# Performance work log

Measured on AMD Instinct MI355X. Metric: run time of the kernel, lower is better.

Reference implementation:

```python
import jax, jax.numpy as jnp
import numpy as np

# Plane-stress elasticity constants (E=1.0, nu=0.3), matching ModelXToResult.__init__
E_MOD = 1.0
NU = 0.3
C11 = E_MOD / (1.0 - NU ** 2)          # = c22
C12 = E_MOD * NU / (1.0 - NU ** 2)     # = c21
C33 = E_MOD / (2.0 * (1.0 + NU))

HIDDEN = 256


def setup_inputs() -> dict:
    key = jax.random.key(0)
    ks = jax.random.split(key, 5)
    B, N = 4, 65536
    X = jax.random.uniform(ks[0], (B, N, 2), dtype=jnp.float32)
    # MLP params (2 -> 256 -> 256 -> 256 -> 2), scaled ~ 1/sqrt(fan_in)
    W1 = jax.random.normal(ks[1], (2, HIDDEN), dtype=jnp.float32) / np.sqrt(2.0)
    b1 = jnp.zeros((HIDDEN,), jnp.float32)
    W2 = jax.random.normal(ks[2], (HIDDEN, HIDDEN), dtype=jnp.float32) / np.sqrt(HIDDEN)
    b2 = jnp.zeros((HIDDEN,), jnp.float32)
    W3 = jax.random.normal(ks[3], (HIDDEN, HIDDEN), dtype=jnp.float32) / np.sqrt(HIDDEN)
    b3 = jnp.zeros((HIDDEN,), jnp.float32)
    Wo = jax.random.normal(ks[4], (HIDDEN, 2), dtype=jnp.float32) / np.sqrt(HIDDEN)
    bo = jnp.zeros((2,), jnp.float32)
    return {"X": X, "W1": W1, "b1": b1, "W2": W2, "b2": b2,
            "W3": W3, "b3": b3, "Wo": Wo, "bo": bo}


def _disp(xy, W1, b1, W2, b2, W3, b3, Wo, bo):
    # xy: [B, N, 2] -> displacement [B, N, 2] = (u, v)
    h = jnp.tanh(xy @ W1 + b1)
    h = jnp.tanh(h @ W2 + b2)
    h = jnp.tanh(h @ W3 + b3)
    return h @ Wo + bo


def reference(X, W1, b1, W2, b2, W3, b3, Wo, bo):
    f = lambda xy: _disp(xy, W1, b1, W2, b2, W3, b3, Wo, bo)
    ones = jnp.ones_like(X[..., 0:1])
    zeros = jnp.zeros_like(ones)
    tx = jnp.concatenate([ones, zeros], axis=-1)  # d/dx tangent
    ty = jnp.concatenate([zeros, ones], axis=-1)  # d/dy tangent
    # Fused forward + full 2x2 Jacobian via two forward-mode JVPs
    out, d_dx = jax.jvp(f, (X,), (tx,))
    _, d_dy = jax.jvp(f, (X,), (ty,))
    u, v = out[..., 0:1], out[..., 1:2]
    u_x, v_x = d_dx[..., 0:1], d_dx[..., 1:2]
    u_y, v_y = d_dy[..., 0:1], d_dy[..., 1:2]
    u_xy = u_y + v_x
    stress_x = C11 * u_x + C12 * v_y
    stress_y = C12 * u_x + C11 * v_y
    stress_xy = C33 * u_xy
    strain_energy_density = 0.5 * (stress_x * u_x + stress_y * v_y + stress_xy * u_xy)
    return (u, v, stress_x, stress_y, stress_xy, strain_energy_density)
```

## Files before the change

### kernel.cpp

```cpp
#include <hip/hip_runtime.h>

#define HIDDEN 256
#define NPTS (4*65536)
#define MTILE 16
#define NWG (NPTS/MTILE)
#define THREADS 256
#define BUF 24576

typedef _Float16 h8  __attribute__((ext_vector_type(8)));
typedef float    f4  __attribute__((ext_vector_type(4)));

__device__ __forceinline__ float2 tanh_ts(float x){
  const float e = exp2f(x * 2.885390081777927f);
  const float r = __builtin_amdgcn_rcpf(e + 1.0f);
  const float t = fmaf(-2.0f, r, 1.0f);
  const float q = 4.0f * r;
  const float s = fmaf(-q, r, q);
  return float2{t, s};
}

__device__ __forceinline__ uint2 pack4(float a, float b, float c, float d){
  uint2 r;
  r.x = __builtin_bit_cast(unsigned int, __builtin_amdgcn_cvt_pkrtz(a, b));
  r.y = __builtin_bit_cast(unsigned int, __builtin_amdgcn_cvt_pkrtz(c, d));
  return r;
}

__device__ __forceinline__ int act_off(int p, int ubyte){
  return p*512 + (ubyte ^ ((p & 15) << 4));
}

__global__ void pack_weights(const float* __restrict__ W, _Float16* __restrict__ dst){
  int i = blockIdx.x * blockDim.x + threadIdx.x;
  int l  = i & 63;
  int nt = (i >> 6) & 15;
  int ks = i >> 10;
  int k0 = ks*32 + ((l >> 4) << 3);
  int n  = nt*16 + (l & 15);
  h8 v;
  #pragma unroll
  for (int j = 0; j < 8; ++j) v[j] = (_Float16)W[(k0 + j)*HIDDEN + n];
  *reinterpret_cast<h8*>(dst + (size_t)i*8) = v;
}

__launch_bounds__(THREADS, 2)
__global__ void pinn_fused(const float* __restrict__ X,
                           const float* __restrict__ W1,
                           const float* __restrict__ b1,
                           const float* __restrict__ b2,
                           const float* __restrict__ b3,
                           const float* __restrict__ Wo,
                           const float* __restrict__ bo,
                           const _Float16* __restrict__ Wp,
                           float* __restrict__ out)
{
  __shared__ __align__(16) char actS[2*BUF];
  __shared__ __align__(16) float partS[MTILE*24];

  const int tid = threadIdx.x;
  const int l   = tid & 63;
  const int lg  = l >> 4;
  const int lr  = l & 15;
  const int Uq  = __builtin_amdgcn_readfirstlane(tid >> 6);

  {
    const int pl = tid & 15;
    const int ug = tid >> 4;
    const int P  = blockIdx.x * MTILE + pl;
    const float2 xy = *reinterpret_cast<const float2*>(X + 2*P);
    #pragma unroll
    for (int c = 0; c < 4; ++c){
      const int u = ug*16 + c*4;
      const f4 w0 = *reinterpret_cast<const f4*>(W1 + u);
      const f4 w1 = *reinterpret_cast<const f4*>(W1 + HIDDEN + u);
      const f4 bb = *reinterpret_cast<const f4*>(b1 + u);
      float h[4], gx[4], gy[4];
      #pragma unroll
      for (int j = 0; j < 4; ++j){
        const float z = fmaf(xy.x, w0[j], fmaf(xy.y, w1[j], bb[j]));
        const float2 ts = tanh_ts(z);
        h[j]  = ts.x;
        gx[j] = ts.y * w0[j];
        gy[j] = ts.y * w1[j];
      }
      const int off = act_off(pl, u*2);
      *reinterpret_cast<uint2*>(actS + 0*8192 + off) = pack4(h[0],h[1],h[2],h[3]);
      *reinterpret_cast<uint2*>(actS + 1*8192 + off) = pack4(gx[0],gx[1],gx[2],gx[3]);
      *reinterpret_cast<uint2*>(actS + 2*8192 + off) = pack4(gy[0],gy[1],gy[2],gy[3]);
    }
  }
  __syncthreads();

  {
    const _Float16* WL = Wp;
    f4 acc[3][4];
    const f4 fzero = {0.f, 0.f, 0.f, 0.f};
    #pragma unroll
    for (int s = 0; s < 3; ++s)
      #pragma unroll
      for (int ut = 0; ut < 4; ++ut) acc[s][ut] = fzero;

    #pragma unroll
    for (int ks = 0; ks < 8; ++ks){
      h8 wf[4];
      #pragma unroll
      for (int ut = 0; ut < 4; ++ut)
        wf[ut] = *reinterpret_cast<const h8*>(WL + (size_t)(((ks*16 + Uq*4 + ut)*64 + l))*8);
      const int off = act_off(lr, ks*64 + lg*16);
      #pragma unroll
      for (int s = 0; s < 3; ++s){
        const h8 af = *reinterpret_cast<const h8*>(actS + s*8192 + off);
        #pragma unroll
        for (int ut = 0; ut < 4; ++ut)
          acc[s][ut] = __builtin_amdgcn_mfma_f32_16x16x32_f16(wf[ut], af, acc[s][ut], 0, 0, 0);
      }
    }

    #pragma unroll
    for (int ut = 0; ut < 4; ++ut){
      const int u0 = Uq*64 + ut*16 + lg*4;
      const f4 bb = *reinterpret_cast<const f4*>(b2 + u0);
      const f4 z  = acc[0][ut];
      const f4 zx = acc[1][ut];
      const f4 zy = acc[2][ut];
      float h[4], gx[4], gy[4];
      #pragma unroll
      for (int j = 0; j < 4; ++j){
        const float2 ts = tanh_ts(z[j] + bb[j]);
        h[j]  = ts.x;
        gx[j] = ts.y * zx[j];
        gy[j] = ts.y * zy[j];
      }
      const int off = act_off(lr, u0*2);
      *reinterpret_cast<uint2*>(actS + BUF + 0*8192 + off) = pack4(h[0],h[1],h[2],h[3]);
      *reinterpret_cast<uint2*>(actS + BUF + 1*8192 + off) = pack4(gx[0],gx[1],gx[2],gx[3]);
      *reinterpret_cast<uint2*>(actS + BUF + 2*8192 + off) = pack4(gy[0],gy[1],gy[2],gy[3]);
    }
  }
  __syncthreads();

  {
    const _Float16* WL = Wp + 65536;
    f4 acc[3][4];
    const f4 fzero = {0.f, 0.f, 0.f, 0.f};
    #pragma unroll
    for (int s = 0; s < 3; ++s)
      #pragma unroll
      for (int ut = 0; ut < 4; ++ut) acc[s][ut] = fzero;

    #pragma unroll
    for (int ks = 0; ks < 8; ++ks){
      h8 wf[4];
      #pragma unroll
      for (int ut = 0; ut < 4; ++ut)
        wf[ut] = *reinterpret_cast<const h8*>(WL + (size_t)(((ks*16 + Uq*4 + ut)*64 + l))*8);
      const int off = act_off(lr, ks*64 + lg*16);
      #pragma unroll
      for (int s = 0; s < 3; ++s){
        const h8 af = *reinterpret_cast<const h8*>(actS + BUF + s*8192 + off);
        #pragma unroll
        for (int ut = 0; ut < 4; ++ut)
          acc[s][ut] = __builtin_amdgcn_mfma_f32_16x16x32_f16(wf[ut], af, acc[s][ut], 0, 0, 0);
      }
    }

    float au=0.f, av=0.f, aux=0.f, avx=0.f, auy=0.f, avy=0.f;
    #pragma unroll
    for (int ut = 0; ut < 4; ++ut){
      const int u0 = Uq*64 + ut*16 + lg*4;
      const f4 bb  = *reinterpret_cast<const f4*>(b3 + u0);
      const f4 wo0 = *reinterpret_cast<const f4*>(Wo + 2*u0);
      const f4 wo1 = *reinterpret_cast<const f4*>(Wo + 2*u0 + 4);
      const f4 z  = acc[0][ut];
      const f4 zx = acc[1][ut];
      const f4 zy = acc[2][ut];
      #pragma unroll
      for (int j = 0; j < 4; ++j){
        const float2 ts = tanh_ts(z[j] + bb[j]);
        const float gx = ts.y * zx[j];
        const float gy = ts.y * zy[j];
        const float wx = (j < 2) ? wo0[2*(j&1)]   : wo1[2*(j&1)];
        const float wy = (j < 2) ? wo0[2*(j&1)+1] : wo1[2*(j&1)+1];
        au  += ts.x*wx;  av  += ts.x*wy;
        aux += gx*wx;    avx += gx*wy;
        auy += gy*wx;    avy += gy*wy;
      }
    }
    #pragma unroll
    for (int m = 16; m <= 32; m <<= 1){
      au  += __shfl_xor(au,  m, 64);
      av  += __shfl_xor(av,  m, 64);
      aux += __shfl_xor(aux, m, 64);
      avx += __shfl_xor(avx, m, 64);
      auy += __shfl_xor(auy, m, 64);
      avy += __shfl_xor(avy, m, 64);
    }
    if (lg == 0){
      float* pp = partS + lr*24 + Uq*6;
      *reinterpret_cast<float2*>(pp + 0) = float2{au,  av };
      *reinterpret_cast<float2*>(pp + 2) = float2{aux, avx};
      *reinterpret_cast<float2*>(pp + 4) = float2{auy, avy};
    }
  }
  __syncthreads();

  if (tid < MTILE){
    const int p = tid;
    const int P = blockIdx.x * MTILE + p;
    float au=0.f, av=0.f, aux=0.f, avx=0.f, auy=0.f, avy=0.f;
    #pragma unroll
    for (int q = 0; q < 4; ++q){
      const float* pp = partS + p*24 + q*6;
      const float2 a = *reinterpret_cast<const float2*>(pp + 0);
      const float2 b = *reinterpret_cast<const float2*>(pp + 2);
      const float2 c = *reinterpret_cast<const float2*>(pp + 4);
      au += a.x; av += a.y; aux += b.x; avx += b.y; auy += c.x; avy += c.y;
    }
    const float C11 = 1.0989010989010988f;
    const float C12 = 0.32967032967032966f;
    const float C33 = 0.38461538461538464f;
    const float u  = au + bo[0];
    const float v  = av + bo[1];
    const float uxy = auy + avx;
    const float sx  = C11*aux + C12*avy;
    const float sy  = C12*aux + C11*avy;
    const float sxy = C33*uxy;
    const float sed = 0.5f*(sx*aux + sy*avy + sxy*uxy);
    out[0*NPTS + P] = u;
    out[1*NPTS + P] = v;
    out[2*NPTS + P] = sx;
    out[3*NPTS + P] = sy;
    out[4*NPTS + P] = sxy;
    out[5*NPTS + P] = sed;
  }
}

extern "C" void kernel_launch(void* const* d_in, const int* in_sizes, int n_in,
                              void* d_out, int out_size, void* d_ws, size_t ws_size,
                              hipStream_t stream)
{
  const float* X  = (const float*)d_in[0];
  const float* W1 = (const float*)d_in[1];
  const float* b1 = (const float*)d_in[2];
  const float* W2 = (const float*)d_in[3];
  const float* b2 = (const float*)d_in[4];
  const float* W3 = (const float*)d_in[5];
  const float* b3 = (const float*)d_in[6];
  const float* Wo = (const float*)d_in[7];
  const float* bo = (const float*)d_in[8];

  _Float16* Wp = (_Float16*)d_ws;

  pack_weights<<<32, 256, 0, stream>>>(W2, Wp);
  pack_weights<<<32, 256, 0, stream>>>(W3, Wp + 65536);
  pinn_fused<<<NWG, THREADS, 0, stream>>>(X, W1, b1, b2, b3, Wo, bo, Wp, (float*)d_out);
}
```

Baseline: 294.4 us.

## Interleave two point tiles per block to overlap MFMA with elementwise phases

Each workgroup now processes two 16-point tiles, staggering them so that one tile's MFMA k-loop runs next to the other tile's tanh/elementwise or layer-1 work between barriers. LDS grows to three activation buffers, and launch bounds drop to one block per SM to leave room for two accumulator sets. The goal is to hide the latency of the elementwise and transcendental work behind matrix-core work within the block. The cost is higher register and LDS pressure and lower occupancy, which may reduce cross-block latency hiding.

```diff
diff --git a/kernel.cpp b/kernel.cpp
--- a/kernel.cpp
+++ b/kernel.cpp
@@ -3,7 +3,8 @@
 #define HIDDEN 256
 #define NPTS (4*65536)
 #define MTILE 16
-#define NWG (NPTS/MTILE)
+#define PPB 32
+#define NWG (NPTS/PPB)
 #define THREADS 256
 #define BUF 24576
 
@@ -43,7 +44,165 @@
   *reinterpret_cast<h8*>(dst + (size_t)i*8) = v;
 }
 
-__launch_bounds__(THREADS, 2)
+
+__device__ __forceinline__ void layer1_phase(int Pbase, const float* __restrict__ X,
+                                             const float* __restrict__ W1,
+                                             const float* __restrict__ b1,
+                                             char* buf, int tid){
+  const int pl = tid & 15;
+  const int ug = tid >> 4;
+  const float2 xy = *reinterpret_cast<const float2*>(X + 2*(Pbase + pl));
+  #pragma unroll
+  for (int c = 0; c < 4; ++c){
+    const int u = ug*16 + c*4;
+    const f4 w0 = *reinterpret_cast<const f4*>(W1 + u);
+    const f4 w1 = *reinterpret_cast<const f4*>(W1 + HIDDEN + u);
+    const f4 bb = *reinterpret_cast<const f4*>(b1 + u);
+    float h[4], gx[4], gy[4];
+    #pragma unroll
+    for (int j = 0; j < 4; ++j){
+      const float z = fmaf(xy.x, w0[j], fmaf(xy.y, w1[j], bb[j]));
+      const float2 ts = tanh_ts(z);
+      h[j]  = ts.x;
+      gx[j] = ts.y * w0[j];
+      gy[j] = ts.y * w1[j];
+    }
+    const int off = act_off(pl, u*2);
+    *reinterpret_cast<uint2*>(buf + 0*8192 + off) = pack4(h[0],h[1],h[2],h[3]);
+    *reinterpret_cast<uint2*>(buf + 1*8192 + off) = pack4(gx[0],gx[1],gx[2],gx[3]);
+    *reinterpret_cast<uint2*>(buf + 2*8192 + off) = pack4(gy[0],gy[1],gy[2],gy[3]);
+  }
+}
+
+__device__ __forceinline__ void kloop_phase(const _Float16* __restrict__ WL,
+                                            const char* buf, f4 (&acc)[3][4],
+                                            int Uq, int l, int lg, int lr){
+  const f4 fzero = {0.f, 0.f, 0.f, 0.f};
+  #pragma unroll
+  for (int s = 0; s < 3; ++s)
+    #pragma unroll
+    for (int ut = 0; ut < 4; ++ut) acc[s][ut] = fzero;
+  #pragma unroll
+  for (int ks = 0; ks < 8; ++ks){
+    h8 wf[4];
+    #pragma unroll
+    for (int ut = 0; ut < 4; ++ut)
+      wf[ut] = *reinterpret_cast<const h8*>(WL + (size_t)(((ks*16 + Uq*4 + ut)*64 + l))*8);
+    const int off = act_off(lr, ks*64 + lg*16);
+    #pragma unroll
+    for (int s = 0; s < 3; ++s){
+      const h8 af = *reinterpret_cast<const h8*>(buf + s*8192 + off);
+      #pragma unroll
+      for (int ut = 0; ut < 4; ++ut)
+        acc[s][ut] = __builtin_amdgcn_mfma_f32_16x16x32_f16(wf[ut], af, acc[s][ut], 0, 0, 0);
+    }
+  }
+}
+
+__device__ __forceinline__ void elem_phase(const f4 (&acc)[3][4],
+                                           const float* __restrict__ bias,
+                                           char* obuf, int Uq, int lg, int lr){
+  #pragma unroll
+  for (int ut = 0; ut < 4; ++ut){
+    const int u0 = Uq*64 + ut*16 + lg*4;
+    const f4 bb = *reinterpret_cast<const f4*>(bias + u0);
+    const f4 z  = acc[0][ut];
+    const f4 zx = acc[1][ut];
+    const f4 zy = acc[2][ut];
+    float h[4], gx[4], gy[4];
+    #pragma unroll
+    for (int j = 0; j < 4; ++j){
+      const float2 ts = tanh_ts(z[j] + bb[j]);
+      h[j]  = ts.x;
+      gx[j] = ts.y * zx[j];
+      gy[j] = ts.y * zy[j];
+    }
+    const int off = act_off(lr, u0*2);
+    *reinterpret_cast<uint2*>(obuf + 0*8192 + off) = pack4(h[0],h[1],h[2],h[3]);
+    *reinterpret_cast<uint2*>(obuf + 1*8192 + off) = pack4(gx[0],gx[1],gx[2],gx[3]);
+    *reinterpret_cast<uint2*>(obuf + 2*8192 + off) = pack4(gy[0],gy[1],gy[2],gy[3]);
+  }
+}
+
+__device__ __forceinline__ void epi_phase(const f4 (&acc)[3][4],
+                                          const float* __restrict__ b3,
+                                          const float* __restrict__ Wo,
+                                          float* __restrict__ partRow,
+                                          int Uq, int lg, int lr){
+  float au=0.f, av=0.f, aux=0.f, avx=0.f, auy=0.f, avy=0.f;
+  #pragma unroll
+  for (int ut = 0; ut < 4; ++ut){
+    const int u0 = Uq*64 + ut*16 + lg*4;
+    const f4 bb  = *reinterpret_cast<const f4*>(b3 + u0);
+    const f4 wo0 = *reinterpret_cast<const f4*>(Wo + 2*u0);
+    const f4 wo1 = *reinterpret_cast<const f4*>(Wo + 2*u0 + 4);
+    const f4 z  = acc[0][ut];
+    const f4 zx = acc[1][ut];
+    const f4 zy = acc[2][ut];
+    #pragma unroll
+    for (int j = 0; j < 4; ++j){
+      const float2 ts = tanh_ts(z[j] + bb[j]);
+      const float gx = ts.y * zx[j];
+      const float gy = ts.y * zy[j];
+      const float wx = (j < 2) ? wo0[2*(j&1)]   : wo1[2*(j&1)];
+      const float wy = (j < 2) ? wo0[2*(j&1)+1] : wo1[2*(j&1)+1];
+      au  += ts.x*wx;  av  += ts.x*wy;
+      aux += gx*wx;    avx += gx*wy;
+      auy += gy*wx;    avy += gy*wy;
+    }
+  }
+  #pragma unroll
+  for (int m = 16; m <= 32; m <<= 1){
+    au  += __shfl_xor(au,  m, 64);
+    av  += __shfl_xor(av,  m, 64);
+    aux += __shfl_xor(aux, m, 64);
+    avx += __shfl_xor(avx, m, 64);
+    auy += __shfl_xor(auy, m, 64);
+    avy += __shfl_xor(avy, m, 64);
+  }
+  if (lg == 0){
+    float* pp = partRow + lr*24 + Uq*6;
+    *reinterpret_cast<float2*>(pp + 0) = float2{au,  av };
+    *reinterpret_cast<float2*>(pp + 2) = float2{aux, avx};
+    *reinterpret_cast<float2*>(pp + 4) = float2{auy, avy};
+  }
+}
+
+__device__ __forceinline__ void final_phase(const float* __restrict__ partRow,
+                                            int Pbase, const float* __restrict__ bo,
+                                            float* __restrict__ out, int tid){
+  if (tid < MTILE){
+    const int p = tid;
+    float au=0.f, av=0.f, aux=0.f, avx=0.f, auy=0.f, avy=0.f;
+    #pragma unroll
+    for (int q = 0; q < 4; ++q){
+      const float* pp = partRow + p*24 + q*6;
+      const float2 a = *reinterpret_cast<const float2*>(pp + 0);
+      const float2 b = *reinterpret_cast<const float2*>(pp + 2);
+      const float2 c = *reinterpret_cast<const float2*>(pp + 4);
+      au += a.x; av += a.y; aux += b.x; avx += b.y; auy += c.x; avy += c.y;
+    }
+    const float C11 = 1.0989010989010988f;
+    const float C12 = 0.32967032967032966f;
+    const float C33 = 0.38461538461538464f;
+    const float u  = au + bo[0];
+    const float v  = av + bo[1];
+    const float uxy = auy + avx;
+    const float sx  = C11*aux + C12*avy;
+    const float sy  = C12*aux + C11*avy;
+    const float sxy = C33*uxy;
+    const float sed = 0.5f*(sx*aux + sy*avy + sxy*uxy);
+    const int P = Pbase + p;
+    out[0*NPTS + P] = u;
+    out[1*NPTS + P] = v;
+    out[2*NPTS + P] = sx;
+    out[3*NPTS + P] = sy;
+    out[4*NPTS + P] = sxy;
+    out[5*NPTS + P] = sed;
+  }
+}
+
+__launch_bounds__(THREADS, 1)
 __global__ void pinn_fused(const float* __restrict__ X,
                            const float* __restrict__ W1,
                            const float* __restrict__ b1,
@@ -54,185 +213,51 @@
                            const _Float16* __restrict__ Wp,
                            float* __restrict__ out)
 {
-  __shared__ __align__(16) char actS[2*BUF];
-  __shared__ __align__(16) float partS[MTILE*24];
-
+  __shared__ __align__(16) char actS[3*BUF];
+  __shared__ __align__(16) float partS[PPB*24];
+
+  char* bufA0 = actS;
+  char* bufA1 = actS + BUF;
+  char* bufB0 = actS + 2*BUF;
+  char* bufB1 = actS;
   const int tid = threadIdx.x;
   const int l   = tid & 63;
   const int lg  = l >> 4;
   const int lr  = l & 15;
   const int Uq  = __builtin_amdgcn_readfirstlane(tid >> 6);
 
-  {
-    const int pl = tid & 15;
-    const int ug = tid >> 4;
-    const int P  = blockIdx.x * MTILE + pl;
-    const float2 xy = *reinterpret_cast<const float2*>(X + 2*P);
-    #pragma unroll
-    for (int c = 0; c < 4; ++c){
-      const int u = ug*16 + c*4;
-      const f4 w0 = *reinterpret_cast<const f4*>(W1 + u);
-      const f4 w1 = *reinterpret_cast<const f4*>(W1 + HIDDEN + u);
-      const f4 bb = *reinterpret_cast<const f4*>(b1 + u);
-      float h[4], gx[4], gy[4];
-      #pragma unroll
-      for (int j = 0; j < 4; ++j){
-        const float z = fmaf(xy.x, w0[j], fmaf(xy.y, w1[j], bb[j]));
-        const float2 ts = tanh_ts(z);
-        h[j]  = ts.x;
-        gx[j] = ts.y * w0[j];
-        gy[j] = ts.y * w1[j];
-      }
-      const int off = act_off(pl, u*2);
-      *reinterpret_cast<uint2*>(actS + 0*8192 + off) = pack4(h[0],h[1],h[2],h[3]);
-      *reinterpret_cast<uint2*>(actS + 1*8192 + off) = pack4(gx[0],gx[1],gx[2],gx[3]);
-      *reinterpret_cast<uint2*>(actS + 2*8192 + off) = pack4(gy[0],gy[1],gy[2],gy[3]);
-    }
-  }
-  __syncthreads();
-
-  {
-    const _Float16* WL = Wp;
-    f4 acc[3][4];
-    const f4 fzero = {0.f, 0.f, 0.f, 0.f};
-    #pragma unroll
-    for (int s = 0; s < 3; ++s)
-      #pragma unroll
-      for (int ut = 0; ut < 4; ++ut) acc[s][ut] = fzero;
-
-    #pragma unroll
-    for (int ks = 0; ks < 8; ++ks){
-      h8 wf[4];
-      #pragma unroll
-      for (int ut = 0; ut < 4; ++ut)
-        wf[ut] = *reinterpret_cast<const h8*>(WL + (size_t)(((ks*16 + Uq*4 + ut)*64 + l))*8);
-      const int off = act_off(lr, ks*64 + lg*16);
-      #pragma unroll
-      for (int s = 0; s < 3; ++s){
-        const h8 af = *reinterpret_cast<const h8*>(actS + s*8192 + off);
-        #pragma unroll
-        for (int ut = 0; ut < 4; ++ut)
-          acc[s][ut] = __builtin_amdgcn_mfma_f32_16x16x32_f16(wf[ut], af, acc[s][ut], 0, 0, 0);
-      }
-    }
-
-    #pragma unroll
-    for (int ut = 0; ut < 4; ++ut){
-      const int u0 = Uq*64 + ut*16 + lg*4;
-      const f4 bb = *reinterpret_cast<const f4*>(b2 + u0);
-      const f4 z  = acc[0][ut];
-      const f4 zx = acc[1][ut];
-      const f4 zy = acc[2][ut];
-      float h[4], gx[4], gy[4];
-      #pragma unroll
-      for (int j = 0; j < 4; ++j){
-        const float2 ts = tanh_ts(z[j] + bb[j]);
-        h[j]  = ts.x;
-        gx[j] = ts.y * zx[j];
-        gy[j] = ts.y * zy[j];
-      }
-      const int off = act_off(lr, u0*2);
-      *reinterpret_cast<uint2*>(actS + BUF + 0*8192 + off) = pack4(h[0],h[1],h[2],h[3]);
-      *reinterpret_cast<uint2*>(actS + BUF + 1*8192 + off) = pack4(gx[0],gx[1],gx[2],gx[3]);
-      *reinterpret_cast<uint2*>(actS + BUF + 2*8192 + off) = pack4(gy[0],gy[1],gy[2],gy[3]);
-    }
-  }
-  __syncthreads();
-
-  {
-    const _Float16* WL = Wp + 65536;
-    f4 acc[3][4];
-    const f4 fzero = {0.f, 0.f, 0.f, 0.f};
-    #pragma unroll
-    for (int s = 0; s < 3; ++s)
-      #pragma unroll
-      for (int ut = 0; ut < 4; ++ut) acc[s][ut] = fzero;
-
-    #pragma unroll
-    for (int ks = 0; ks < 8; ++ks){
-      h8 wf[4];
-      #pragma unroll
-      for (int ut = 0; ut < 4; ++ut)
-        wf[ut] = *reinterpret_cast<const h8*>(WL + (size_t)(((ks*16 + Uq*4 + ut)*64 + l))*8);
-      const int off = act_off(lr, ks*64 + lg*16);
-      #pragma unroll
-      for (int s = 0; s < 3; ++s){
-        const h8 af = *reinterpret_cast<const h8*>(actS + BUF + s*8192 + off);
-        #pragma unroll
-        for (int ut = 0; ut < 4; ++ut)
-          acc[s][ut] = __builtin_amdgcn_mfma_f32_16x16x32_f16(wf[ut], af, acc[s][ut], 0, 0, 0);
-      }
-    }
-
-    float au=0.f, av=0.f, aux=0.f, avx=0.f, auy=0.f, avy=0.f;
-    #pragma unroll
-    for (int ut = 0; ut < 4; ++ut){
-      const int u0 = Uq*64 + ut*16 + lg*4;
-      const f4 bb  = *reinterpret_cast<const f4*>(b3 + u0);
-      const f4 wo0 = *reinterpret_cast<const f4*>(Wo + 2*u0);
-      const f4 wo1 = *reinterpret_cast<const f4*>(Wo + 2*u0 + 4);
-      const f4 z  = acc[0][ut];
-      const f4 zx = acc[1][ut];
-      const f4 zy = acc[2][ut];
-      #pragma unroll
-      for (int j = 0; j < 4; ++j){
-        const float2 ts = tanh_ts(z[j] + bb[j]);
-        const float gx = ts.y * zx[j];
-        const float gy = ts.y * zy[j];
-        const float wx = (j < 2) ? wo0[2*(j&1)]   : wo1[2*(j&1)];
-        const float wy = (j < 2) ? wo0[2*(j&1)+1] : wo1[2*(j&1)+1];
-        au  += ts.x*wx;  av  += ts.x*wy;
-        aux += gx*wx;    avx += gx*wy;
-        auy += gy*wx;    avy += gy*wy;
-      }
-    }
-    #pragma unroll
-    for (int m = 16; m <= 32; m <<= 1){
-      au  += __shfl_xor(au,  m, 64);
-      av  += __shfl_xor(av,  m, 64);
-      aux += __shfl_xor(aux, m, 64);
-      avx += __shfl_xor(avx, m, 64);
-      auy += __shfl_xor(auy, m, 64);
-      avy += __shfl_xor(avy, m, 64);
-    }
-    if (lg == 0){
-      float* pp = partS + lr*24 + Uq*6;
-      *reinterpret_cast<float2*>(pp + 0) = float2{au,  av };
-      *reinterpret_cast<float2*>(pp + 2) = float2{aux, avx};
-      *reinterpret_cast<float2*>(pp + 4) = float2{auy, avy};
-    }
-  }
-  __syncthreads();
-
-  if (tid < MTILE){
-    const int p = tid;
-    const int P = blockIdx.x * MTILE + p;
-    float au=0.f, av=0.f, aux=0.f, avx=0.f, auy=0.f, avy=0.f;
-    #pragma unroll
-    for (int q = 0; q < 4; ++q){
-      const float* pp = partS + p*24 + q*6;
-      const float2 a = *reinterpret_cast<const float2*>(pp + 0);
-      const float2 b = *reinterpret_cast<const float2*>(pp + 2);
-      const float2 c = *reinterpret_cast<const float2*>(pp + 4);
-      au += a.x; av += a.y; aux += b.x; avx += b.y; auy += c.x; avy += c.y;
-    }
-    const float C11 = 1.0989010989010988f;
-    const float C12 = 0.32967032967032966f;
-    const float C33 = 0.38461538461538464f;
-    const float u  = au + bo[0];
-    const float v  = av + bo[1];
-    const float uxy = auy + avx;
-    const float sx  = C11*aux + C12*avy;
-    const float sy  = C12*aux + C11*avy;
-    const float sxy = C33*uxy;
-    const float sed = 0.5f*(sx*aux + sy*avy + sxy*uxy);
-    out[0*NPTS + P] = u;
-    out[1*NPTS + P] = v;
-    out[2*NPTS + P] = sx;
-    out[3*NPTS + P] = sy;
-    out[4*NPTS + P] = sxy;
-    out[5*NPTS + P] = sed;
-  }
+  const int PA = blockIdx.x * PPB;
+  const int PB = PA + MTILE;
+  const _Float16* W2p = Wp;
+  const _Float16* W3p = Wp + 65536;
+
+  f4 accA[3][4];
+  f4 accB[3][4];
+
+  layer1_phase(PA, X, W1, b1, bufA0, tid);
+  __syncthreads();
+
+  kloop_phase(W2p, bufA0, accA, Uq, l, lg, lr);
+  layer1_phase(PB, X, W1, b1, bufB0, tid);
+  __syncthreads();
+
+  kloop_phase(W2p, bufB0, accB, Uq, l, lg, lr);
+  elem_phase(accA, b2, bufA1, Uq, lg, lr);
+  __syncthreads();
+
+  kloop_phase(W3p, bufA1, accA, Uq, l, lg, lr);
+  elem_phase(accB, b2, bufB1, Uq, lg, lr);
+  __syncthreads();
+
+  kloop_phase(W3p, bufB1, accB, Uq, l, lg, lr);
+  epi_phase(accA, b3, Wo, partS, Uq, lg, lr);
+  __syncthreads();
+
+  epi_phase(accB, b3, Wo, partS + MTILE*24, Uq, lg, lr);
+  final_phase(partS, PA, bo, out, tid);
+  __syncthreads();
+
+  final_phase(partS + MTILE*24, PB, bo, out, tid);
 }
 
 extern "C" void kernel_launch(void* const* d_in, const int* in_sizes, int n_in,
```

Result: slower. 406.7 us (+38.1%).
